# Kernel optimization log

Measured on AMD Instinct MI355X. Metric: run time of the kernel, lower is better.

Reference implementation:

```python
import jax, jax.numpy as jnp
import numpy as np

DIM = 512
H = 8
HD = DIM // H
MAX_DIST = 128
TABLE = (2 * MAX_DIST + 1) ** 2
LAMBDA_INIT = 0.8


def setup_inputs() -> dict:
    key = jax.random.key(0)
    ks = jax.random.split(key, 20)
    B, Nq, Nkv = 4, 1024, 1024
    inp = {
        "x_q": jax.random.normal(ks[0], (B, Nq, DIM), jnp.float32),
        "x_kv": jax.random.normal(ks[1], (B, Nkv, DIM), jnp.float32),
        "coords_q": jax.random.randint(ks[2], (B, Nq, 2), 0, 256, jnp.int32),
        "coords_k": jax.random.randint(ks[3], (B, Nkv, 2), 0, 256, jnp.int32),
        "alpha_map": jax.random.uniform(ks[4], (B, Nq, 1), jnp.float32),
        "Wq": jax.random.normal(ks[5], (DIM, DIM), jnp.float32) * 0.02,
        "bq": jnp.zeros((DIM,), jnp.float32),
        "Wk": jax.random.normal(ks[6], (DIM, DIM), jnp.float32) * 0.02,
        "bk": jnp.zeros((DIM,), jnp.float32),
        "Wv": jax.random.normal(ks[7], (DIM, DIM), jnp.float32) * 0.02,
        "bv": jnp.zeros((DIM,), jnp.float32),
        "lambda_q1": jax.random.normal(ks[8], (H // 2, HD), jnp.float32) * 0.1,
        "lambda_k1": jax.random.normal(ks[9], (H // 2, HD), jnp.float32) * 0.1,
        "lambda_q2": jax.random.normal(ks[10], (H // 2, HD), jnp.float32) * 0.1,
        "lambda_k2": jax.random.normal(ks[11], (H // 2, HD), jnp.float32) * 0.1,
        "rpe_table": jax.random.normal(ks[12], (TABLE, H), jnp.float32) * 0.02,
        "Wp": jax.random.normal(ks[13], (DIM, DIM), jnp.float32) * 0.02,
        "bp": jnp.zeros((DIM,), jnp.float32),
    }
    return inp


def reference(x_q, x_kv, coords_q, coords_k, alpha_map,
              Wq, bq, Wk, bk, Wv, bv,
              lambda_q1, lambda_k1, lambda_q2, lambda_k2,
              rpe_table, Wp, bp):
    B, Nq, C = x_q.shape
    Nkv = x_kv.shape[1]
    n_half = H // 2
    scale = HD ** -0.5

    # projections -> [B, H, N, HD]
    q = (x_q @ Wq.T + bq).reshape(B, Nq, H, HD).transpose(0, 2, 1, 3)
    k = (x_kv @ Wk.T + bk).reshape(B, Nkv, H, HD).transpose(0, 2, 1, 3)
    v = (x_kv @ Wv.T + bv).reshape(B, Nkv, H, HD).transpose(0, 2, 1, 3)

    # sparse relative position bias: gather per-pair from table
    rel = coords_q[:, :, None, :] - coords_k[:, None, :, :] + MAX_DIST  # [B,Nq,Nkv,2]
    rel = jnp.clip(rel, 0, 2 * MAX_DIST)
    idx = rel[..., 0] * (2 * MAX_DIST + 1) + rel[..., 1]  # [B,Nq,Nkv]
    bias = rpe_table[idx].transpose(0, 3, 1, 2)  # [B,H,Nq,Nkv]

    scores = jnp.einsum('bhqd,bhkd->bhqk', q, k) * scale + bias
    probs = jax.nn.softmax(scores, axis=-1)
    x_std = jnp.einsum('bhqk,bhkd->bhqd', probs, v)

    lam1 = jnp.exp(jnp.sum(lambda_q1 * lambda_k1, axis=-1))  # [n_half]
    lam2 = jnp.exp(jnp.sum(lambda_q2 * lambda_k2, axis=-1))
    lam = (lam1 - lam2 + LAMBDA_INIT)[None, :, None, None]

    attn_diff = probs[:, :n_half] - lam * probs[:, n_half:]
    x_diff = jnp.einsum('bhqk,bhkd->bhqd', attn_diff, v[:, :n_half])

    alpha = alpha_map[:, None]  # [B,1,Nq,1]
    x1 = x_std[:, :n_half] + alpha * x_diff
    x = jnp.concatenate([x1, x_std[:, n_half:]], axis=1)  # [B,H,Nq,HD]
    x = x.transpose(0, 2, 1, 3).reshape(B, Nq, C)
    return x @ Wp.T + bp
```

## Files before the change

### kernel.cpp

```cpp
#include <hip/hip_runtime.h>
#include <cstddef>
#include <cstdint>

#define DIM   512
#define NSEQ  1024
#define NB    4

typedef unsigned short u16;
typedef short bf16x8 __attribute__((ext_vector_type(8)));
typedef _Float16 half8v __attribute__((ext_vector_type(8)));
typedef float f32x4  __attribute__((ext_vector_type(4)));

#define MFMA(a, b, c)  __builtin_amdgcn_mfma_f32_16x16x32_bf16(a, b, c, 0, 0, 0)
#define MFMAH(a, b, c) __builtin_amdgcn_mfma_f32_16x16x32_f16(a, b, c, 0, 0, 0)

__device__ inline void split2(float x, u16& h, u16& l) {
  unsigned u = __float_as_uint(x);
  unsigned hb = (u + 0x7fffu + ((u >> 16) & 1u)) >> 16;
  float fh = __uint_as_float(hb << 16);
  float r = x - fh;
  unsigned v = __float_as_uint(r);
  unsigned lb = (v + 0x7fffu + ((v >> 16) & 1u)) >> 16;
  h = (u16)hb; l = (u16)lb;
}

__device__ inline uint2 pack4(const u16 a[4]) {
  return make_uint2((unsigned)a[0] | ((unsigned)a[1] << 16),
                    (unsigned)a[2] | ((unsigned)a[3] << 16));
}

__device__ inline uint4 pack8(const u16 a[8]) {
  return make_uint4((unsigned)a[0] | ((unsigned)a[1] << 16),
                    (unsigned)a[2] | ((unsigned)a[3] << 16),
                    (unsigned)a[4] | ((unsigned)a[5] << 16),
                    (unsigned)a[6] | ((unsigned)a[7] << 16));
}

__device__ inline u16 f2h(float x) {
  _Float16 h = (_Float16)x;
  u16 r; __builtin_memcpy(&r, &h, 2);
  return r;
}
__device__ inline float h2f(u16 b) {
  _Float16 h; __builtin_memcpy(&h, &b, 2);
  return (float)h;
}
__device__ inline unsigned pkh2(float a, float b) {
  return (unsigned)f2h(a) | ((unsigned)f2h(b) << 16);
}

__global__ __launch_bounds__(256) void split_w4(
    const float* __restrict__ w0, const float* __restrict__ w1,
    const float* __restrict__ w2, const float* __restrict__ w3,
    u16* __restrict__ out) {
  const int y = blockIdx.y;
  const float* src = (y == 0) ? w0 : (y == 1) ? w1 : (y == 2) ? w2 : w3;
  u16* o0 = out + (size_t)y * 524288;
  const int e = (blockIdx.x * 256 + threadIdx.x) * 4;
  const int m = e >> 9, c = e & 511;
  const float4 v = *(const float4*)(src + e);
  u16 h[4], l[4];
  split2(v.x, h[0], l[0]); split2(v.y, h[1], l[1]);
  split2(v.z, h[2], l[2]); split2(v.w, h[3], l[3]);
  u16* o = o0 + (size_t)m * 1024 + c;
  *(uint2*)o = pack4(h);
  *(uint2*)(o + 512) = pack4(l);
}

#define GLDS(g, l)                                                        \
  __builtin_amdgcn_global_load_lds(                                       \
      (const __attribute__((address_space(1))) void*)(g),                 \
      (__attribute__((address_space(3))) void*)(l), 16, 0, 0)

__global__ __launch_bounds__(256) void rpebuild(
    const int* __restrict__ cq, const int* __restrict__ ck,
    const float* __restrict__ rpe, u16* __restrict__ biasT) {
  __shared__ u16 Ts[8 * 16 * 64];
  const int t = threadIdx.x;
  const int q0 = blockIdx.x * 64, k0 = blockIdx.y * 16, b = blockIdx.z;
  const int qn = t & 63, kb = t >> 6;
  const int2 cqv = ((const int2*)cq)[b * NSEQ + q0 + qn];
#pragma unroll
  for (int j = 0; j < 4; ++j) {
    const int k = kb * 4 + j;
    const int2 ckv = ((const int2*)ck)[b * NSEQ + k0 + k];
    const int r0 = min(max(cqv.x - ckv.x + 128, 0), 256);
    const int r1 = min(max(cqv.y - ckv.y + 128, 0), 256);
    const float* rp = rpe + (size_t)(r0 * 257 + r1) * 8;
    const float4 f0 = *(const float4*)rp;
    const float4 f1 = *(const float4*)(rp + 4);
    u16* dst = Ts + k * 64 + qn;
    dst[0 * 1024] = f2h(f0.x); dst[1 * 1024] = f2h(f0.y);
    dst[2 * 1024] = f2h(f0.z); dst[3 * 1024] = f2h(f0.w);
    dst[4 * 1024] = f2h(f1.x); dst[5 * 1024] = f2h(f1.y);
    dst[6 * 1024] = f2h(f1.z); dst[7 * 1024] = f2h(f1.w);
  }
  __syncthreads();
#pragma unroll
  for (int i = 0; i < 4; ++i) {
    const int e = i * 256 + t;
    const int row = e >> 3, c8 = e & 7;
    const int hh = row >> 4, k = row & 15;
    const uint4 v = *(const uint4*)(Ts + row * 64 + c8 * 8);
    *(uint4*)(biasT + ((size_t)(b * 8 + hh) * 1024 + k0 + k) * 1024 +
              q0 + c8 * 8) = v;
  }
}

template <int A_SPLIT, int OUT_MODE>
__device__ __forceinline__ void gemm_body(
    u16* __restrict__ Ah, u16* __restrict__ Al,
    u16* __restrict__ Bh, u16* __restrict__ Bl,
    const void* __restrict__ Ap, const u16* __restrict__ B2,
    const float* __restrict__ bias, void* __restrict__ outp,
    float scale, int m0, int n0) {
  const int tid = threadIdx.x;
  const int lane = tid & 63, w = tid >> 6;
  const int wm = (w & 1) * 32, wn = (w >> 1) * 32;

  const int sr  = w * 16 + (lane >> 3);
  const int scg = (lane & 7) ^ (sr & 7);
  const size_t bR = (size_t)(n0 + sr) * 1024 + scg * 8;
  const u16* gBh0 = B2 + bR;        const u16* gBh1 = B2 + bR + 8192;
  const u16* gBl0 = B2 + bR + 512;  const u16* gBl1 = B2 + bR + 8704;
  char* lBh = (char*)Bh + w * 2048; char* lBl = (char*)Bl + w * 2048;

  const u16* gAh0 = nullptr; const u16* gAh1 = nullptr;
  const u16* gAl0 = nullptr; const u16* gAl1 = nullptr;
  char* lAh = (char*)Ah + w * 2048; char* lAl = (char*)Al + w * 2048;
  const float* Af = nullptr;
  int arow = 0, apos0 = 0, apos1 = 0;
  if (A_SPLIT) {
    const size_t aR = (size_t)(m0 + sr) * 1024 + scg * 8;
    gAh0 = (const u16*)Ap + aR; gAh1 = gAh0 + 8192;
    gAl0 = gAh0 + 512;          gAl1 = gAh0 + 8704;
  } else {
    arow = tid >> 2;
    const int acg = tid & 3;
    Af = (const float*)Ap + (size_t)(m0 + arow) * 512 + acg * 8;
    apos0 = (acg ^ (arow & 7)) * 8;
    apos1 = ((acg + 4) ^ (arow & 7)) * 8;
  }

  const int fr = lane & 15, kq = lane >> 4, fx = lane & 7;
  int aoff[2][2], boff[2][2];
#pragma unroll
  for (int s = 0; s < 2; ++s)
#pragma unroll
    for (int t = 0; t < 2; ++t) {
      aoff[s][t] = (wm + t * 16 + fr) * 64 + (((s * 4 + kq) ^ fx)) * 8;
      boff[s][t] = (wn + t * 16 + fr) * 64 + (((s * 4 + kq) ^ fx)) * 8;
    }

  f32x4 acc[2][2] = {};
  for (int k0 = 0; k0 < 512; k0 += 64) {
    float4 f0, f1, f2, f3;
    if (!A_SPLIT) {
      f0 = *(const float4*)(Af + k0);
      f1 = *(const float4*)(Af + k0 + 4);
      f2 = *(const float4*)(Af + k0 + 32);
      f3 = *(const float4*)(Af + k0 + 36);
    }
    __syncthreads();
    GLDS(gBh0 + k0, lBh); GLDS(gBh1 + k0, lBh + 1024);
    GLDS(gBl0 + k0, lBl); GLDS(gBl1 + k0, lBl + 1024);
    if (A_SPLIT) {
      GLDS(gAh0 + k0, lAh); GLDS(gAh1 + k0, lAh + 1024);
      GLDS(gAl0 + k0, lAl); GLDS(gAl1 + k0, lAl + 1024);
    } else {
      u16 h8[8], l8[8];
      split2(f0.x, h8[0], l8[0]); split2(f0.y, h8[1], l8[1]);
      split2(f0.z, h8[2], l8[2]); split2(f0.w, h8[3], l8[3]);
      split2(f1.x, h8[4], l8[4]); split2(f1.y, h8[5], l8[5]);
      split2(f1.z, h8[6], l8[6]); split2(f1.w, h8[7], l8[7]);
      *(uint4*)(Ah + arow * 64 + apos0) = pack8(h8);
      *(uint4*)(Al + arow * 64 + apos0) = pack8(l8);
      split2(f2.x, h8[0], l8[0]); split2(f2.y, h8[1], l8[1]);
      split2(f2.z, h8[2], l8[2]); split2(f2.w, h8[3], l8[3]);
      split2(f3.x, h8[4], l8[4]); split2(f3.y, h8[5], l8[5]);
      split2(f3.z, h8[6], l8[6]); split2(f3.w, h8[7], l8[7]);
      *(uint4*)(Ah + arow * 64 + apos1) = pack8(h8);
      *(uint4*)(Al + arow * 64 + apos1) = pack8(l8);
    }
    __syncthreads();
#pragma unroll
    for (int s = 0; s < 2; ++s) {
      bf16x8 ah[2], al[2], bh[2], bl[2];
#pragma unroll
      for (int t = 0; t < 2; ++t) {
        ah[t] = *(const bf16x8*)(Ah + aoff[s][t]);
        al[t] = *(const bf16x8*)(Al + aoff[s][t]);
        bh[t] = *(const bf16x8*)(Bh + boff[s][t]);
        bl[t] = *(const bf16x8*)(Bl + boff[s][t]);
      }
#pragma unroll
      for (int i = 0; i < 2; ++i)
#pragma unroll
        for (int j = 0; j < 2; ++j) {
          acc[i][j] = MFMA(al[i], bh[j], acc[i][j]);
          acc[i][j] = MFMA(ah[i], bl[j], acc[i][j]);
          acc[i][j] = MFMA(ah[i], bh[j], acc[i][j]);
        }
    }
  }

  const int er = (lane >> 4) * 4, ec = lane & 15;
#pragma unroll
  for (int i = 0; i < 2; ++i)
#pragma unroll
    for (int j = 0; j < 2; ++j) {
      const int row = m0 + wm + i * 16 + er;
      const int col = n0 + wn + j * 16 + ec;
      const float bv = bias[col];
      if (OUT_MODE == 4) {
        u16 hf[4];
#pragma unroll
        for (int r = 0; r < 4; ++r) hf[r] = f2h(acc[i][j][r] + bv);
        const int bb = row >> 10, kk = row & 1023;
        *(uint2*)((u16*)outp + ((size_t)(bb * 512 + col)) * 1024 + kk) =
            pack4(hf);
      } else {
#pragma unroll
        for (int r = 0; r < 4; ++r) {
          const float v = (acc[i][j][r] + bv) * scale;
          if (OUT_MODE == 3) {
            ((u16*)outp)[(size_t)(row + r) * 512 + col] = f2h(v);
          } else {
            ((float*)outp)[(size_t)(row + r) * 512 + col] = v;
          }
        }
      }
    }
}

__global__ __launch_bounds__(256) void gemm_qkv(
    const float* __restrict__ xq, const float* __restrict__ xkv,
    const u16* __restrict__ w2, const float* __restrict__ bq,
    const float* __restrict__ bk, const float* __restrict__ bv,
    u16* __restrict__ q2f, u16* __restrict__ k2f, u16* __restrict__ vtf) {
  __shared__ __align__(16) u16 Ah[4096], Al[4096], Bh[4096], Bl[4096];
  const int z = blockIdx.z;
  const float* A = (z == 0) ? xq : xkv;
  const u16* B = w2 + (size_t)z * 524288;
  const int m0 = blockIdx.y * 64, n0 = blockIdx.x * 64;
  if (z == 2) {
    gemm_body<0, 4>(Ah, Al, Bh, Bl, A, B, bv, vtf, 1.0f, m0, n0);
  } else if (z == 1) {
    gemm_body<0, 3>(Ah, Al, Bh, Bl, A, B, bk, k2f, 1.0f, m0, n0);
  } else {
    gemm_body<0, 3>(Ah, Al, Bh, Bl, A, B, bq, q2f, 0.125f, m0, n0);
  }
}

__global__ __launch_bounds__(256) void gemm_out(
    const u16* __restrict__ xa2, const u16* __restrict__ w2p,
    const float* __restrict__ bp, float* __restrict__ out) {
  __shared__ __align__(16) u16 Ah[4096], Al[4096], Bh[4096], Bl[4096];
  gemm_body<1, 0>(Ah, Al, Bh, Bl, xa2, w2p, bp, out, 1.0f,
                  blockIdx.y * 64, blockIdx.x * 64);
}

__global__ __launch_bounds__(256) void attn_f16(
    const u16* __restrict__ q2f, const u16* __restrict__ k2f,
    const u16* __restrict__ vtf, const float* __restrict__ amap,
    const float* __restrict__ lq1, const float* __restrict__ lk1,
    const float* __restrict__ lq2, const float* __restrict__ lk2,
    const u16* __restrict__ biasT, u16* __restrict__ xo) {
  __shared__ __align__(16) u16 KsL[2][4096];
  __shared__ __align__(16) u16 VtL[2][4096];
  __shared__ float lam_s;

  const int tid = threadIdx.x;
  const int lane = tid & 63, w = tid >> 6;
  const int h = w >> 1, qs = w & 1;
  const int hp = blockIdx.y, b = blockIdx.z;
  const int q0 = blockIdx.x * 32;
  const int head = hp + 4 * h;
  const int lq = lane & 15, lg = lane >> 4;
  const int q = qs * 16 + lq;
  const size_t qrow = (size_t)(b * NSEQ + q0 + q);

  if (tid < 64) {
    float p1 = lq1[hp * 64 + tid] * lk1[hp * 64 + tid];
    float p2 = lq2[hp * 64 + tid] * lk2[hp * 64 + tid];
#pragma unroll
    for (int m = 32; m >= 1; m >>= 1) {
      p1 += __shfl_xor(p1, m, 64);
      p2 += __shfl_xor(p2, m, 64);
    }
    if (tid == 0) lam_s = __expf(p1) - __expf(p2) + 0.8f;
  }

  const float alpha = amap[qrow];

  half8v Qf[2];
#pragma unroll
  for (int ks = 0; ks < 2; ++ks)
    Qf[ks] = *(const half8v*)(q2f + qrow * 512 + head * 64 + ks * 32 + lg * 8);

  f32x4 Ya[4] = {};
  f32x4 Yb[4] = {};
  float m_run = -1e30f, l_run = 0.0f;

  const int lr = lane >> 3, pc = lane & 7;
  const int lc = pc ^ lr;
  const int cw = w * 2;

  auto stage = [&](int it, int p) {
#pragma unroll
    for (int i = 0; i < 2; ++i) {
      const int c = cw + i;
      const int row = c * 8 + lr;
      const int sh = row >> 5, k = row & 31;
      const u16* src = k2f + (size_t)(b * NSEQ + it * 32 + k) * 512 +
                       (hp + 4 * sh) * 64 + lc * 8;
      GLDS(src, (char*)KsL[p] + c * 1024);
    }
#pragma unroll
    for (int i = 0; i < 2; ++i) {
      const int c = cw + i;
      const int d = c * 8 + lr;
      const int hv = lc >> 2, kc = lc & 3;
      const u16* src = vtf + (size_t)(b * 512 + (hp + 4 * hv) * 64 + d) * 1024 +
                       it * 32 + kc * 8;
      GLDS(src, (char*)VtL[p] + c * 1024);
    }
  };

  const u16* bT = biasT + ((size_t)(b * 8 + head) << 20) + q0 + q;

  stage(0, 0);

  for (int it = 0; it < 32; ++it) {
    const int p = it & 1;
    __syncthreads();
    if (it + 1 < 32) stage(it + 1, p ^ 1);

    u16 rb[8];
    {
      const u16* bt = bT + (size_t)(it * 32) * 1024;
#pragma unroll
      for (int kt = 0; kt < 2; ++kt)
#pragma unroll
        for (int r = 0; r < 4; ++r)
          rb[kt * 4 + r] = bt[(size_t)(kt * 16 + lg * 4 + r) * 1024];
    }

    const u16* Kb = KsL[p];
    f32x4 st[2] = {};
#pragma unroll
    for (int kt = 0; kt < 2; ++kt) {
      const int krow = kt * 16 + lq;
      const int rx = krow & 7;
#pragma unroll
      for (int ks = 0; ks < 2; ++ks) {
        const int phys = (ks * 4 + lg) ^ rx;
        const half8v kf = *(const half8v*)(Kb + (h * 32 + krow) * 64 + phys * 8);
        st[kt] = MFMAH(kf, Qf[ks], st[kt]);
      }
    }

    float sv[2][4];
    float mx = -1e30f;
#pragma unroll
    for (int kt = 0; kt < 2; ++kt)
#pragma unroll
      for (int r = 0; r < 4; ++r) {
        const float s = st[kt][r] + h2f(rb[kt * 4 + r]);
        sv[kt][r] = s;
        mx = fmaxf(mx, s);
      }
    mx = fmaxf(mx, __shfl_xor(mx, 16, 64));
    mx = fmaxf(mx, __shfl_xor(mx, 32, 64));
    const float mnew = fmaxf(m_run, mx);
    const float a = __expf(m_run - mnew);
    m_run = mnew;
    float pr[2][4], ps = 0.0f;
#pragma unroll
    for (int kt = 0; kt < 2; ++kt)
#pragma unroll
      for (int r = 0; r < 4; ++r) {
        pr[kt][r] = __expf(sv[kt][r] - mnew);
        ps += pr[kt][r];
      }
    ps += __shfl_xor(ps, 16, 64);
    ps += __shfl_xor(ps, 32, 64);
    l_run = l_run * a + ps;
#pragma unroll
    for (int dt = 0; dt < 4; ++dt) Ya[dt] *= a;
    if (h == 1) {
#pragma unroll
      for (int dt = 0; dt < 4; ++dt) Yb[dt] *= a;
    }

    const unsigned a0 = pkh2(pr[0][0], pr[0][1]);
    const unsigned a1 = pkh2(pr[0][2], pr[0][3]);
    const unsigned b0 = pkh2(pr[1][0], pr[1][1]);
    const unsigned b1 = pkh2(pr[1][2], pr[1][3]);
    const int srcA = lq + ((lg & 1) << 5);
    const unsigned A0 = __shfl((int)a0, srcA),      A1 = __shfl((int)a1, srcA);
    const unsigned B0 = __shfl((int)b0, srcA),      B1 = __shfl((int)b1, srcA);
    const unsigned C0 = __shfl((int)a0, srcA + 16), C1 = __shfl((int)a1, srcA + 16);
    const unsigned D0 = __shfl((int)b0, srcA + 16), D1 = __shfl((int)b1, srcA + 16);
    const bool t2 = lg >= 2;
    const uint4 Pu = make_uint4(t2 ? B0 : A0, t2 ? B1 : A1,
                                t2 ? D0 : C0, t2 ? D1 : C1);
    half8v pb;
    __builtin_memcpy(&pb, &Pu, 16);

    const u16* Vb = VtL[p];
    if (h == 0) {
#pragma unroll
      for (int dt = 0; dt < 4; ++dt) {
        const int d = dt * 16 + lq;
        const half8v v1 = *(const half8v*)(Vb + d * 64 + ((lg ^ (d & 7))) * 8);
        Ya[dt] = MFMAH(v1, pb, Ya[dt]);
      }
    } else {
#pragma unroll
      for (int dt = 0; dt < 4; ++dt) {
        const int d = dt * 16 + lq;
        const int dx = d & 7;
        const half8v v1 = *(const half8v*)(Vb + d * 64 + ((lg ^ dx)) * 8);
        Yb[dt] = MFMAH(v1, pb, Yb[dt]);
        const half8v v2 = *(const half8v*)(Vb + d * 64 + (((4 + lg) ^ dx)) * 8);
        Ya[dt] = MFMAH(v2, pb, Ya[dt]);
      }
    }
  }

  __syncthreads();
  float* y2x = (float*)VtL;
  float* l2s = (float*)KsL;
  if (h == 1) {
    if (lane < 16) l2s[qs * 16 + lane] = l_run;
#pragma unroll
    for (int dt = 0; dt < 4; ++dt)
#pragma unroll
      for (int r = 0; r < 4; ++r)
        y2x[(qs * 64 + lane) * 16 + dt * 4 + r] = Yb[dt][r];
  }
  __syncthreads();
  if (h == 1) {
    const float inv2 = 1.0f / l_run;
#pragma unroll
    for (int dt = 0; dt < 4; ++dt) {
      u16 hh[4], ll[4];
#pragma unroll
      for (int r = 0; r < 4; ++r) split2(Ya[dt][r] * inv2, hh[r], ll[r]);
      u16* o = xo + qrow * 1024 + (hp + 4) * 64 + dt * 16 + lg * 4;
      *(uint2*)o = pack4(hh);
      *(uint2*)(o + 512) = pack4(ll);
    }
  } else {
    const float inv1 = 1.0f / l_run;
    const float inv2 = 1.0f / l2s[qs * 16 + lq];
    const float c1 = (1.0f + alpha) * inv1;
    const float c2 = alpha * lam_s * inv2;
#pragma unroll
    for (int dt = 0; dt < 4; ++dt) {
      u16 hh[4], ll[4];
#pragma unroll
      for (int r = 0; r < 4; ++r) {
        const float y2 = y2x[(qs * 64 + lane) * 16 + dt * 4 + r];
        split2(c1 * Ya[dt][r] - c2 * y2, hh[r], ll[r]);
      }
      u16* o = xo + qrow * 1024 + hp * 64 + dt * 16 + lg * 4;
      *(uint2*)o = pack4(hh);
      *(uint2*)(o + 512) = pack4(ll);
    }
  }
}

extern "C" void kernel_launch(void* const* d_in, const int* in_sizes, int n_in,
                              void* d_out, int out_size, void* d_ws, size_t ws_size,
                              hipStream_t stream) {
  const float* x_q   = (const float*)d_in[0];
  const float* x_kv  = (const float*)d_in[1];
  const int*   c_q   = (const int*)d_in[2];
  const int*   c_k   = (const int*)d_in[3];
  const float* alpha = (const float*)d_in[4];
  const float* Wq    = (const float*)d_in[5];
  const float* bq    = (const float*)d_in[6];
  const float* Wk    = (const float*)d_in[7];
  const float* bk    = (const float*)d_in[8];
  const float* Wv    = (const float*)d_in[9];
  const float* bv    = (const float*)d_in[10];
  const float* lq1   = (const float*)d_in[11];
  const float* lk1   = (const float*)d_in[12];
  const float* lq2   = (const float*)d_in[13];
  const float* lk2   = (const float*)d_in[14];
  const float* rpe   = (const float*)d_in[15];
  const float* Wp    = (const float*)d_in[16];
  const float* bp    = (const float*)d_in[17];

  u16* w2    = (u16*)d_ws;
  u16* q2f   = (u16*)((char*)d_ws + (4u << 20));
  u16* k2f   = (u16*)((char*)d_ws + (8u << 20));
  u16* vtf   = (u16*)((char*)d_ws + (12u << 20));
  u16* xa    = (u16*)((char*)d_ws + (16u << 20));
  u16* biasT = (u16*)((char*)d_ws + (28u << 20));

  split_w4<<<dim3(256, 4), 256, 0, stream>>>(Wq, Wk, Wv, Wp, w2);
  rpebuild<<<dim3(16, 64, 4), 256, 0, stream>>>(c_q, c_k, rpe, biasT);
  gemm_qkv<<<dim3(8, 64, 3), 256, 0, stream>>>(x_q, x_kv, w2, bq, bk, bv,
                                               q2f, k2f, vtf);
  attn_f16<<<dim3(32, 4, NB), 256, 0, stream>>>(
      q2f, k2f, vtf, alpha, lq1, lk1, lq2, lk2, biasT, xa);
  gemm_out<<<dim3(8, 64), 256, 0, stream>>>(xa, w2 + 3 * 524288, bp,
                                            (float*)d_out);
}
```

Before: 230.3 us.

## Pre-split activations, enlarge GEMM tiles, use exp2 softmax, split attention by head-dim

Activations are split to bf16 hi/lo in a separate pass so both GEMMs load A through direct global-to-LDS copies. The GEMM tile grows to 128x64 with a 3-blocks-per-CU launch bound. Softmax switches to exp2 by folding log2(e) into the Q scale and the RPE bias. Attention now uses 16-query blocks, with the warps splitting the value head dimension, which doubles the grid. The extra split pass adds memory traffic and uses the output buffer as scratch for the split x_kv.

Result: slower. 246.1 us (+6.8%).

```diff
diff --git a/kernel.cpp b/kernel.cpp
--- a/kernel.cpp
+++ b/kernel.cpp
@@ -5,6 +5,7 @@
 #define DIM   512
 #define NSEQ  1024
 #define NB    4
+#define LOG2E 1.44269504f
 
 typedef unsigned short u16;
 typedef short bf16x8 __attribute__((ext_vector_type(8)));
@@ -29,13 +30,6 @@
                     (unsigned)a[2] | ((unsigned)a[3] << 16));
 }
 
-__device__ inline uint4 pack8(const u16 a[8]) {
-  return make_uint4((unsigned)a[0] | ((unsigned)a[1] << 16),
-                    (unsigned)a[2] | ((unsigned)a[3] << 16),
-                    (unsigned)a[4] | ((unsigned)a[5] << 16),
-                    (unsigned)a[6] | ((unsigned)a[7] << 16));
-}
-
 __device__ inline u16 f2h(float x) {
   _Float16 h = (_Float16)x;
   u16 r; __builtin_memcpy(&r, &h, 2);
@@ -47,6 +41,19 @@
 }
 __device__ inline unsigned pkh2(float a, float b) {
   return (unsigned)f2h(a) | ((unsigned)f2h(b) << 16);
+}
+
+__device__ inline void split_body(const float* __restrict__ in,
+                                  u16* __restrict__ out, int e4) {
+  const int e = e4 * 4;
+  const int m = e >> 9, c = e & 511;
+  const float4 v = *(const float4*)(in + e);
+  u16 h[4], l[4];
+  split2(v.x, h[0], l[0]); split2(v.y, h[1], l[1]);
+  split2(v.z, h[2], l[2]); split2(v.w, h[3], l[3]);
+  u16* o = out + (size_t)m * 1024 + c;
+  *(uint2*)o = pack4(h);
+  *(uint2*)(o + 512) = pack4(l);
 }
 
 __global__ __launch_bounds__(256) void split_w4(
@@ -55,16 +62,15 @@
     u16* __restrict__ out) {
   const int y = blockIdx.y;
   const float* src = (y == 0) ? w0 : (y == 1) ? w1 : (y == 2) ? w2 : w3;
-  u16* o0 = out + (size_t)y * 524288;
-  const int e = (blockIdx.x * 256 + threadIdx.x) * 4;
-  const int m = e >> 9, c = e & 511;
-  const float4 v = *(const float4*)(src + e);
-  u16 h[4], l[4];
-  split2(v.x, h[0], l[0]); split2(v.y, h[1], l[1]);
-  split2(v.z, h[2], l[2]); split2(v.w, h[3], l[3]);
-  u16* o = o0 + (size_t)m * 1024 + c;
-  *(uint2*)o = pack4(h);
-  *(uint2*)(o + 512) = pack4(l);
+  split_body(src, out + (size_t)y * 524288, blockIdx.x * 256 + threadIdx.x);
+}
+
+__global__ __launch_bounds__(256) void split_x(
+    const float* __restrict__ xq, const float* __restrict__ xkv,
+    u16* __restrict__ xq2, u16* __restrict__ xkv2) {
+  const float* src = blockIdx.y ? xkv : xq;
+  u16* dst = blockIdx.y ? xkv2 : xq2;
+  split_body(src, dst, blockIdx.x * 256 + threadIdx.x);
 }
 
 #define GLDS(g, l)                                                        \
@@ -90,10 +96,10 @@
     const float4 f0 = *(const float4*)rp;
     const float4 f1 = *(const float4*)(rp + 4);
     u16* dst = Ts + k * 64 + qn;
-    dst[0 * 1024] = f2h(f0.x); dst[1 * 1024] = f2h(f0.y);
-    dst[2 * 1024] = f2h(f0.z); dst[3 * 1024] = f2h(f0.w);
-    dst[4 * 1024] = f2h(f1.x); dst[5 * 1024] = f2h(f1.y);
-    dst[6 * 1024] = f2h(f1.z); dst[7 * 1024] = f2h(f1.w);
+    dst[0 * 1024] = f2h(f0.x * LOG2E); dst[1 * 1024] = f2h(f0.y * LOG2E);
+    dst[2 * 1024] = f2h(f0.z * LOG2E); dst[3 * 1024] = f2h(f0.w * LOG2E);
+    dst[4 * 1024] = f2h(f1.x * LOG2E); dst[5 * 1024] = f2h(f1.y * LOG2E);
+    dst[6 * 1024] = f2h(f1.z * LOG2E); dst[7 * 1024] = f2h(f1.w * LOG2E);
   }
   __syncthreads();
 #pragma unroll
@@ -107,94 +113,65 @@
   }
 }
 
-template <int A_SPLIT, int OUT_MODE>
-__device__ __forceinline__ void gemm_body(
+template <int OUT_MODE>
+__device__ __forceinline__ void gemm128(
     u16* __restrict__ Ah, u16* __restrict__ Al,
     u16* __restrict__ Bh, u16* __restrict__ Bl,
-    const void* __restrict__ Ap, const u16* __restrict__ B2,
+    const u16* __restrict__ A2, const u16* __restrict__ B2,
     const float* __restrict__ bias, void* __restrict__ outp,
     float scale, int m0, int n0) {
   const int tid = threadIdx.x;
   const int lane = tid & 63, w = tid >> 6;
-  const int wm = (w & 1) * 32, wn = (w >> 1) * 32;
-
-  const int sr  = w * 16 + (lane >> 3);
-  const int scg = (lane & 7) ^ (sr & 7);
-  const size_t bR = (size_t)(n0 + sr) * 1024 + scg * 8;
-  const u16* gBh0 = B2 + bR;        const u16* gBh1 = B2 + bR + 8192;
-  const u16* gBl0 = B2 + bR + 512;  const u16* gBl1 = B2 + bR + 8704;
-  char* lBh = (char*)Bh + w * 2048; char* lBl = (char*)Bl + w * 2048;
-
-  const u16* gAh0 = nullptr; const u16* gAh1 = nullptr;
-  const u16* gAl0 = nullptr; const u16* gAl1 = nullptr;
-  char* lAh = (char*)Ah + w * 2048; char* lAl = (char*)Al + w * 2048;
-  const float* Af = nullptr;
-  int arow = 0, apos0 = 0, apos1 = 0;
-  if (A_SPLIT) {
-    const size_t aR = (size_t)(m0 + sr) * 1024 + scg * 8;
-    gAh0 = (const u16*)Ap + aR; gAh1 = gAh0 + 8192;
-    gAl0 = gAh0 + 512;          gAl1 = gAh0 + 8704;
-  } else {
-    arow = tid >> 2;
-    const int acg = tid & 3;
-    Af = (const float*)Ap + (size_t)(m0 + arow) * 512 + acg * 8;
-    apos0 = (acg ^ (arow & 7)) * 8;
-    apos1 = ((acg + 4) ^ (arow & 7)) * 8;
-  }
-
-  const int fr = lane & 15, kq = lane >> 4, fx = lane & 7;
-  int aoff[2][2], boff[2][2];
-#pragma unroll
-  for (int s = 0; s < 2; ++s)
-#pragma unroll
-    for (int t = 0; t < 2; ++t) {
-      aoff[s][t] = (wm + t * 16 + fr) * 64 + (((s * 4 + kq) ^ fx)) * 8;
-      boff[s][t] = (wn + t * 16 + fr) * 64 + (((s * 4 + kq) ^ fx)) * 8;
-    }
-
-  f32x4 acc[2][2] = {};
+  const int wm = (w & 1) * 64, wn = (w >> 1) * 32;
+  const int lr = lane >> 3;
+  const int scc = (lane & 7) ^ lr;
+
+  const u16* gA = A2 + (size_t)(m0 + w * 32 + lr) * 1024 + scc * 8;
+  const u16* gB = B2 + (size_t)(n0 + w * 16 + lr) * 1024 + scc * 8;
+  char* lAh = (char*)Ah + w * 4096;  char* lAl = (char*)Al + w * 4096;
+  char* lBh = (char*)Bh + w * 2048;  char* lBl = (char*)Bl + w * 2048;
+
+  const int fr = lane & 15, kq = lane >> 4, fx = fr & 7;
+  int aoff[2][4], boff[2][2];
+#pragma unroll
+  for (int s = 0; s < 2; ++s) {
+#pragma unroll
+    for (int i = 0; i < 4; ++i)
+      aoff[s][i] = (wm + i * 16 + fr) * 64 + (((s * 4 + kq) ^ fx)) * 8;
+#pragma unroll
+    for (int j = 0; j < 2; ++j)
+      boff[s][j] = (wn + j * 16 + fr) * 64 + (((s * 4 + kq) ^ fx)) * 8;
+  }
+
+  f32x4 acc[4][2] = {};
   for (int k0 = 0; k0 < 512; k0 += 64) {
-    float4 f0, f1, f2, f3;
-    if (!A_SPLIT) {
-      f0 = *(const float4*)(Af + k0);
-      f1 = *(const float4*)(Af + k0 + 4);
-      f2 = *(const float4*)(Af + k0 + 32);
-      f3 = *(const float4*)(Af + k0 + 36);
-    }
     __syncthreads();
-    GLDS(gBh0 + k0, lBh); GLDS(gBh1 + k0, lBh + 1024);
-    GLDS(gBl0 + k0, lBl); GLDS(gBl1 + k0, lBl + 1024);
-    if (A_SPLIT) {
-      GLDS(gAh0 + k0, lAh); GLDS(gAh1 + k0, lAh + 1024);
-      GLDS(gAl0 + k0, lAl); GLDS(gAl1 + k0, lAl + 1024);
-    } else {
-      u16 h8[8], l8[8];
-      split2(f0.x, h8[0], l8[0]); split2(f0.y, h8[1], l8[1]);
-      split2(f0.z, h8[2], l8[2]); split2(f0.w, h8[3], l8[3]);
-      split2(f1.x, h8[4], l8[4]); split2(f1.y, h8[5], l8[5]);
-      split2(f1.z, h8[6], l8[6]); split2(f1.w, h8[7], l8[7]);
-      *(uint4*)(Ah + arow * 64 + apos0) = pack8(h8);
-      *(uint4*)(Al + arow * 64 + apos0) = pack8(l8);
-      split2(f2.x, h8[0], l8[0]); split2(f2.y, h8[1], l8[1]);
-      split2(f2.z, h8[2], l8[2]); split2(f2.w, h8[3], l8[3]);
-      split2(f3.x, h8[4], l8[4]); split2(f3.y, h8[5], l8[5]);
-      split2(f3.z, h8[6], l8[6]); split2(f3.w, h8[7], l8[7]);
-      *(uint4*)(Ah + arow * 64 + apos1) = pack8(h8);
-      *(uint4*)(Al + arow * 64 + apos1) = pack8(l8);
+#pragma unroll
+    for (int i = 0; i < 4; ++i) {
+      GLDS(gA + (size_t)i * 8192 + k0, lAh + i * 1024);
+      GLDS(gA + (size_t)i * 8192 + 512 + k0, lAl + i * 1024);
+    }
+#pragma unroll
+    for (int i = 0; i < 2; ++i) {
+      GLDS(gB + (size_t)i * 8192 + k0, lBh + i * 1024);
+      GLDS(gB + (size_t)i * 8192 + 512 + k0, lBl + i * 1024);
     }
     __syncthreads();
 #pragma unroll
     for (int s = 0; s < 2; ++s) {
-      bf16x8 ah[2], al[2], bh[2], bl[2];
-#pragma unroll
-      for (int t = 0; t < 2; ++t) {
-        ah[t] = *(const bf16x8*)(Ah + aoff[s][t]);
-        al[t] = *(const bf16x8*)(Al + aoff[s][t]);
-        bh[t] = *(const bf16x8*)(Bh + boff[s][t]);
-        bl[t] = *(const bf16x8*)(Bl + boff[s][t]);
-      }
-#pragma unroll
-      for (int i = 0; i < 2; ++i)
+      bf16x8 ah[4], al[4], bh[2], bl[2];
+#pragma unroll
+      for (int i = 0; i < 4; ++i) {
+        ah[i] = *(const bf16x8*)(Ah + aoff[s][i]);
+        al[i] = *(const bf16x8*)(Al + aoff[s][i]);
+      }
+#pragma unroll
+      for (int j = 0; j < 2; ++j) {
+        bh[j] = *(const bf16x8*)(Bh + boff[s][j]);
+        bl[j] = *(const bf16x8*)(Bl + boff[s][j]);
+      }
+#pragma unroll
+      for (int i = 0; i < 4; ++i)
 #pragma unroll
         for (int j = 0; j < 2; ++j) {
           acc[i][j] = MFMA(al[i], bh[j], acc[i][j]);
@@ -206,7 +183,7 @@
 
   const int er = (lane >> 4) * 4, ec = lane & 15;
 #pragma unroll
-  for (int i = 0; i < 2; ++i)
+  for (int i = 0; i < 4; ++i)
 #pragma unroll
     for (int j = 0; j < 2; ++j) {
       const int row = m0 + wm + i * 16 + er;
@@ -215,7 +192,7 @@
       if (OUT_MODE == 4) {
         u16 hf[4];
 #pragma unroll
-        for (int r = 0; r < 4; ++r) hf[r] = f2h(acc[i][j][r] + bv);
+        for (int r = 0; r < 4; ++r) hf[r] = f2h((acc[i][j][r] + bv) * scale);
         const int bb = row >> 10, kk = row & 1023;
         *(uint2*)((u16*)outp + ((size_t)(bb * 512 + col)) * 1024 + kk) =
             pack4(hf);
@@ -223,41 +200,37 @@
 #pragma unroll
         for (int r = 0; r < 4; ++r) {
           const float v = (acc[i][j][r] + bv) * scale;
-          if (OUT_MODE == 3) {
+          if (OUT_MODE == 3)
             ((u16*)outp)[(size_t)(row + r) * 512 + col] = f2h(v);
-          } else {
+          else
             ((float*)outp)[(size_t)(row + r) * 512 + col] = v;
-          }
         }
       }
     }
 }
 
-__global__ __launch_bounds__(256) void gemm_qkv(
-    const float* __restrict__ xq, const float* __restrict__ xkv,
+__global__ __launch_bounds__(256, 3) void gemm_qkv(
+    const u16* __restrict__ xq2, const u16* __restrict__ xkv2,
     const u16* __restrict__ w2, const float* __restrict__ bq,
     const float* __restrict__ bk, const float* __restrict__ bv,
     u16* __restrict__ q2f, u16* __restrict__ k2f, u16* __restrict__ vtf) {
-  __shared__ __align__(16) u16 Ah[4096], Al[4096], Bh[4096], Bl[4096];
+  __shared__ __align__(16) u16 Ah[8192], Al[8192], Bh[4096], Bl[4096];
   const int z = blockIdx.z;
-  const float* A = (z == 0) ? xq : xkv;
-  const u16* B = w2 + (size_t)z * 524288;
-  const int m0 = blockIdx.y * 64, n0 = blockIdx.x * 64;
-  if (z == 2) {
-    gemm_body<0, 4>(Ah, Al, Bh, Bl, A, B, bv, vtf, 1.0f, m0, n0);
-  } else if (z == 1) {
-    gemm_body<0, 3>(Ah, Al, Bh, Bl, A, B, bk, k2f, 1.0f, m0, n0);
-  } else {
-    gemm_body<0, 3>(Ah, Al, Bh, Bl, A, B, bq, q2f, 0.125f, m0, n0);
-  }
-}
-
-__global__ __launch_bounds__(256) void gemm_out(
+  const int m0 = blockIdx.x * 128, n0 = blockIdx.y * 64;
+  if (z == 0)
+    gemm128<3>(Ah, Al, Bh, Bl, xq2, w2, bq, q2f, 0.125f * LOG2E, m0, n0);
+  else if (z == 1)
+    gemm128<3>(Ah, Al, Bh, Bl, xkv2, w2 + 524288, bk, k2f, 1.0f, m0, n0);
+  else
+    gemm128<4>(Ah, Al, Bh, Bl, xkv2, w2 + 2 * 524288, bv, vtf, 1.0f, m0, n0);
+}
+
+__global__ __launch_bounds__(256, 3) void gemm_out(
     const u16* __restrict__ xa2, const u16* __restrict__ w2p,
     const float* __restrict__ bp, float* __restrict__ out) {
-  __shared__ __align__(16) u16 Ah[4096], Al[4096], Bh[4096], Bl[4096];
-  gemm_body<1, 0>(Ah, Al, Bh, Bl, xa2, w2p, bp, out, 1.0f,
-                  blockIdx.y * 64, blockIdx.x * 64);
+  __shared__ __align__(16) u16 Ah[8192], Al[8192], Bh[4096], Bl[4096];
+  gemm128<0>(Ah, Al, Bh, Bl, xa2, w2p, bp, out, 1.0f,
+             blockIdx.x * 128, blockIdx.y * 64);
 }
 
 __global__ __launch_bounds__(256) void attn_f16(
@@ -272,13 +245,12 @@
 
   const int tid = threadIdx.x;
   const int lane = tid & 63, w = tid >> 6;
-  const int h = w >> 1, qs = w & 1;
+  const int h = w >> 1, dv = w & 1;
   const int hp = blockIdx.y, b = blockIdx.z;
-  const int q0 = blockIdx.x * 32;
+  const int q0 = blockIdx.x * 16;
   const int head = hp + 4 * h;
   const int lq = lane & 15, lg = lane >> 4;
-  const int q = qs * 16 + lq;
-  const size_t qrow = (size_t)(b * NSEQ + q0 + q);
+  const size_t qrow = (size_t)(b * NSEQ + q0 + lq);
 
   if (tid < 64) {
     float p1 = lq1[hp * 64 + tid] * lk1[hp * 64 + tid];
@@ -298,12 +270,12 @@
   for (int ks = 0; ks < 2; ++ks)
     Qf[ks] = *(const half8v*)(q2f + qrow * 512 + head * 64 + ks * 32 + lg * 8);
 
-  f32x4 Ya[4] = {};
-  f32x4 Yb[4] = {};
+  f32x4 Ya[2] = {};
+  f32x4 Yb[2] = {};
   float m_run = -1e30f, l_run = 0.0f;
 
-  const int lr = lane >> 3, pc = lane & 7;
-  const int lc = pc ^ lr;
+  const int lr = lane >> 3;
+  const int lc = (lane & 7) ^ lr;
   const int cw = w * 2;
 
   auto stage = [&](int it, int p) {
@@ -327,7 +299,7 @@
     }
   };
 
-  const u16* bT = biasT + ((size_t)(b * 8 + head) << 20) + q0 + q;
+  const u16* bT = biasT + ((size_t)(b * 8 + head) << 20) + q0 + lq;
 
   stage(0, 0);
 
@@ -373,25 +345,21 @@
     mx = fmaxf(mx, __shfl_xor(mx, 16, 64));
     mx = fmaxf(mx, __shfl_xor(mx, 32, 64));
     const float mnew = fmaxf(m_run, mx);
-    const float a = __expf(m_run - mnew);
+    const float a = exp2f(m_run - mnew);
     m_run = mnew;
     float pr[2][4], ps = 0.0f;
 #pragma unroll
     for (int kt = 0; kt < 2; ++kt)
 #pragma unroll
       for (int r = 0; r < 4; ++r) {
-        pr[kt][r] = __expf(sv[kt][r] - mnew);
+        pr[kt][r] = exp2f(sv[kt][r] - mnew);
         ps += pr[kt][r];
       }
     ps += __shfl_xor(ps, 16, 64);
     ps += __shfl_xor(ps, 32, 64);
     l_run = l_run * a + ps;
-#pragma unroll
-    for (int dt = 0; dt < 4; ++dt) Ya[dt] *= a;
-    if (h == 1) {
-#pragma unroll
-      for (int dt = 0; dt < 4; ++dt) Yb[dt] *= a;
-    }
+    Ya[0] *= a; Ya[1] *= a;
+    if (h == 1) { Yb[0] *= a; Yb[1] *= a; }
 
     const unsigned a0 = pkh2(pr[0][0], pr[0][1]);
     const unsigned a1 = pkh2(pr[0][2], pr[0][3]);
@@ -411,15 +379,15 @@
     const u16* Vb = VtL[p];
     if (h == 0) {
 #pragma unroll
-      for (int dt = 0; dt < 4; ++dt) {
-        const int d = dt * 16 + lq;
+      for (int dt = 0; dt < 2; ++dt) {
+        const int d = dv * 32 + dt * 16 + lq;
         const half8v v1 = *(const half8v*)(Vb + d * 64 + ((lg ^ (d & 7))) * 8);
         Ya[dt] = MFMAH(v1, pb, Ya[dt]);
       }
     } else {
 #pragma unroll
-      for (int dt = 0; dt < 4; ++dt) {
-        const int d = dt * 16 + lq;
+      for (int dt = 0; dt < 2; ++dt) {
+        const int d = dv * 32 + dt * 16 + lq;
         const int dx = d & 7;
         const half8v v1 = *(const half8v*)(Vb + d * 64 + ((lg ^ dx)) * 8);
         Yb[dt] = MFMAH(v1, pb, Yb[dt]);
@@ -433,39 +401,39 @@
   float* y2x = (float*)VtL;
   float* l2s = (float*)KsL;
   if (h == 1) {
-    if (lane < 16) l2s[qs * 16 + lane] = l_run;
-#pragma unroll
-    for (int dt = 0; dt < 4; ++dt)
+    if (dv == 0 && lane < 16) l2s[lane] = l_run;
+#pragma unroll
+    for (int dt = 0; dt < 2; ++dt)
 #pragma unroll
       for (int r = 0; r < 4; ++r)
-        y2x[(qs * 64 + lane) * 16 + dt * 4 + r] = Yb[dt][r];
+        y2x[(dv * 64 + lane) * 8 + dt * 4 + r] = Yb[dt][r];
   }
   __syncthreads();
   if (h == 1) {
     const float inv2 = 1.0f / l_run;
 #pragma unroll
-    for (int dt = 0; dt < 4; ++dt) {
+    for (int dt = 0; dt < 2; ++dt) {
       u16 hh[4], ll[4];
 #pragma unroll
       for (int r = 0; r < 4; ++r) split2(Ya[dt][r] * inv2, hh[r], ll[r]);
-      u16* o = xo + qrow * 1024 + (hp + 4) * 64 + dt * 16 + lg * 4;
+      u16* o = xo + qrow * 1024 + (hp + 4) * 64 + dv * 32 + dt * 16 + lg * 4;
       *(uint2*)o = pack4(hh);
       *(uint2*)(o + 512) = pack4(ll);
     }
   } else {
     const float inv1 = 1.0f / l_run;
-    const float inv2 = 1.0f / l2s[qs * 16 + lq];
+    const float inv2 = 1.0f / l2s[lq];
     const float c1 = (1.0f + alpha) * inv1;
     const float c2 = alpha * lam_s * inv2;
 #pragma unroll
-    for (int dt = 0; dt < 4; ++dt) {
+    for (int dt = 0; dt < 2; ++dt) {
       u16 hh[4], ll[4];
 #pragma unroll
       for (int r = 0; r < 4; ++r) {
-        const float y2 = y2x[(qs * 64 + lane) * 16 + dt * 4 + r];
+        const float y2 = y2x[(dv * 64 + lane) * 8 + dt * 4 + r];
         split2(c1 * Ya[dt][r] - c2 * y2, hh[r], ll[r]);
       }
-      u16* o = xo + qrow * 1024 + hp * 64 + dt * 16 + lg * 4;
+      u16* o = xo + qrow * 1024 + hp * 64 + dv * 32 + dt * 16 + lg * 4;
       *(uint2*)o = pack4(hh);
       *(uint2*)(o + 512) = pack4(ll);
     }
@@ -495,18 +463,21 @@
   const float* bp    = (const float*)d_in[17];
 
   u16* w2    = (u16*)d_ws;
-  u16* q2f   = (u16*)((char*)d_ws + (4u << 20));
-  u16* k2f   = (u16*)((char*)d_ws + (8u << 20));
-  u16* vtf   = (u16*)((char*)d_ws + (12u << 20));
-  u16* xa    = (u16*)((char*)d_ws + (16u << 20));
+  u16* xq2   = (u16*)((char*)d_ws + (4u << 20));
+  u16* q2f   = (u16*)((char*)d_ws + (12u << 20));
+  u16* k2f   = (u16*)((char*)d_ws + (16u << 20));
+  u16* vtf   = (u16*)((char*)d_ws + (20u << 20));
+  u16* xa    = xq2;
   u16* biasT = (u16*)((char*)d_ws + (28u << 20));
+  u16* xkv2  = (u16*)d_out;
 
   split_w4<<<dim3(256, 4), 256, 0, stream>>>(Wq, Wk, Wv, Wp, w2);
+  split_x<<<dim3(2048, 2), 256, 0, stream>>>(x_q, x_kv, xq2, xkv2);
   rpebuild<<<dim3(16, 64, 4), 256, 0, stream>>>(c_q, c_k, rpe, biasT);
-  gemm_qkv<<<dim3(8, 64, 3), 256, 0, stream>>>(x_q, x_kv, w2, bq, bk, bv,
+  gemm_qkv<<<dim3(32, 8, 3), 256, 0, stream>>>(xq2, xkv2, w2, bq, bk, bv,
                                                q2f, k2f, vtf);
-  attn_f16<<<dim3(32, 4, NB), 256, 0, stream>>>(
+  attn_f16<<<dim3(64, 4, NB), 256, 0, stream>>>(
       q2f, k2f, vtf, alpha, lq1, lk1, lq2, lk2, biasT, xa);
-  gemm_out<<<dim3(8, 64), 256, 0, stream>>>(xa, w2 + 3 * 524288, bp,
+  gemm_out<<<dim3(32, 8), 256, 0, stream>>>(xa, w2 + 3 * 524288, bp,
                                             (float*)d_out);
 }
```
